# Optimization experiments

Measured on AMD Instinct MI355X. Metric: run time of the kernel, lower is better.

## Reference

```python
import jax, jax.numpy as jnp
import numpy as np

N_NODES = 50000
N_EDGES = 1_600_000
IN_DIM = 256
OUT_DIM = 128
NEG_SLOPE = 0.01  # F.leaky_relu default


def setup_inputs() -> dict:
    key = jax.random.key(0)
    k1, k2, k3, k4, k5 = jax.random.split(key, 5)
    x = jax.random.normal(k1, (N_NODES, IN_DIM), dtype=jnp.float32)
    # glorot_init: uniform in [-r, r], r = sqrt(6/(in+out))
    r = np.sqrt(6.0 / (IN_DIM + OUT_DIM)).astype(np.float32)
    weight = jax.random.uniform(k2, (IN_DIM, OUT_DIM), dtype=jnp.float32, minval=-r, maxval=r)
    adj_rows = jax.random.randint(k3, (N_EDGES,), 0, N_NODES, dtype=jnp.int64 if jax.config.jax_enable_x64 else jnp.int32)
    adj_cols = jax.random.randint(k4, (N_EDGES,), 0, N_NODES, dtype=jnp.int64 if jax.config.jax_enable_x64 else jnp.int32)
    adj_vals = jax.random.uniform(k5, (N_EDGES,), dtype=jnp.float32)
    return {"x": x, "weight": weight, "adj_vals": adj_vals,
            "adj_rows": adj_rows, "adj_cols": adj_cols}


def reference(x, weight, adj_vals, adj_rows, adj_cols):
    # h = X @ W : [N, OUT_DIM]
    h = x @ weight
    # sparse adj @ h via edge-list SpMM: out[r] += v * h[c]
    msgs = adj_vals[:, None] * h[adj_cols]            # [E, OUT_DIM]
    agg = jax.ops.segment_sum(msgs, adj_rows, num_segments=N_NODES)
    # leaky_relu epilogue
    return jnp.where(agg >= 0, agg, NEG_SLOPE * agg)
```

## Files before the change

kernel.cpp:

```cpp
#include <hip/hip_runtime.h>
#include <hip/hip_fp16.h>

#define N_NODES 50000
#define N_EDGES 1600000
#define IN_DIM 256
#define OUT_DIM 128
#define NEG_SLOPE 0.01f

#define SB_SH     10
#define NSB       49
#define BIN_SH    5
#define BIN_ROWS  32
#define NBIN_PAD  (NSB * 32)
#define NPART     8
#define ECAP      4608
#define SEGP      256
#define CAPG      (NPART * SEGP)
#define OVF_CAP   65536

#define SCAT_BLOCKS 256
#define EPB_S (N_EDGES / SCAT_BLOCKS)
#define SCAT_ITERS ((EPB_S + 511) / 512)

#define BM 128
#define GEMM_BLOCKS ((N_NODES + BM - 1) / BM)
#define PREP_BLOCKS (SCAT_BLOCKS + GEMM_BLOCKS + 1)

typedef _Float16 f16x8 __attribute__((ext_vector_type(8)));
typedef float    f32x4 __attribute__((ext_vector_type(4)));
typedef float    f32x8 __attribute__((ext_vector_type(8)));

__device__ __forceinline__ float lrelu(float v) {
    return v >= 0.f ? v : NEG_SLOPE * v;
}

#define CVT16(lo, hi) do { \
    lo[0]=(_Float16)xr[0].x; lo[1]=(_Float16)xr[0].y; lo[2]=(_Float16)xr[0].z; lo[3]=(_Float16)xr[0].w; \
    lo[4]=(_Float16)xr[1].x; lo[5]=(_Float16)xr[1].y; lo[6]=(_Float16)xr[1].z; lo[7]=(_Float16)xr[1].w; \
    hi[0]=(_Float16)xr[2].x; hi[1]=(_Float16)xr[2].y; hi[2]=(_Float16)xr[2].z; hi[3]=(_Float16)xr[2].w; \
    hi[4]=(_Float16)xr[3].x; hi[5]=(_Float16)xr[3].y; hi[6]=(_Float16)xr[3].z; hi[7]=(_Float16)xr[3].w; \
} while (0)

__global__ __launch_bounds__(512, 2) void prep(const int* __restrict__ rows,
                                               const int* __restrict__ cols,
                                               const float* __restrict__ vals,
                                               const float* __restrict__ x,
                                               const float* __restrict__ w,
                                               int* __restrict__ cstartarr,
                                               int* __restrict__ ovfcnt,
                                               int2* __restrict__ cbuf,
                                               __half* __restrict__ h) {
    __shared__ __attribute__((aligned(16))) char smem[50432];
    const int bid = blockIdx.x;
    const int t   = threadIdx.x;

    if (bid >= SCAT_BLOCKS + GEMM_BLOCKS) {
        if (t == 0) *ovfcnt = 0;
        return;
    }

    if (bid < SCAT_BLOCKS) {
        int2* lsort  = (int2*)smem;
        int*  hist   = (int*)(smem + 50000);
        int*  cstart = (int*)(smem + 50200);
        const int lane  = t & 63;
        const int blk   = bid;
        const int ebase = blk * EPB_S;

        if (t < NSB) hist[t] = 0;
        __syncthreads();

        int myr[SCAT_ITERS];
#pragma unroll
        for (int k = 0; k < SCAT_ITERS; ++k) {
            const int i = k * 512 + t;
            myr[k] = -1;
            if (i < EPB_S) {
                myr[k] = rows[ebase + i];
                atomicAdd(&hist[myr[k] >> SB_SH], 1);
            }
        }
        __syncthreads();

        if (t < 64) {
            const int v = (t < NSB) ? hist[t] : 0;
            int s = v;
#pragma unroll
            for (int off = 1; off < 64; off <<= 1) {
                const int u = __shfl_up(s, off);
                if (lane >= off) s += u;
            }
            if (t < NSB) { cstart[t] = s - v; hist[t] = s - v; }
        }
        __syncthreads();

#pragma unroll
        for (int k = 0; k < SCAT_ITERS; ++k) {
            const int i = k * 512 + t;
            if (i < EPB_S) {
                const int e = ebase + i;
                const int r = myr[k];
                const int pos = atomicAdd(&hist[r >> SB_SH], 1);
                lsort[pos] = make_int2((int)(((unsigned)r << 16) | (unsigned)cols[e]),
                                       __float_as_int(vals[e]));
            }
        }
        __syncthreads();

        {
            const int4* src = (const int4*)lsort;
            int4* dst = (int4*)(cbuf + (size_t)blk * EPB_S);
            for (int i = t; i < EPB_S / 2; i += 512) dst[i] = src[i];
        }
        if (t < NSB)  cstartarr[blk * 50 + t]   = cstart[t];
        if (t == NSB) cstartarr[blk * 50 + NSB] = EPB_S;
        return;
    }

    f16x8* wt8h = (f16x8*)smem;
    f16x8* xs8  = (f16x8*)(smem + 32768);
    const int a256 = (t < 256);
    const int lane = t & 63;
    const int wv   = t >> 6;
    const int row0 = (bid - SCAT_BLOCKS) * BM;

    const int srow = t >> 1;
    const int skh  = t & 1;
    const int grow = row0 + srow;
    const bool rv  = a256 && (grow < N_NODES);
    const float* xp = x + (size_t)(rv ? grow : 0) * IN_DIM + skh * 16;

    float4 xr[4];
    if (a256) {
#pragma unroll
        for (int i = 0; i < 4; ++i)
            xr[i] = rv ? ((const float4*)xp)[i] : make_float4(0.f, 0.f, 0.f, 0.f);
        f16x8 lo, hi;
        CVT16(lo, hi);
        xs8[(0 * 4 + skh * 2 + 0) * 128 + srow] = lo;
        xs8[(0 * 4 + skh * 2 + 1) * 128 + srow] = hi;
    }
    __syncthreads();

    f32x4 acc[2][8];
#pragma unroll
    for (int mf = 0; mf < 2; ++mf)
#pragma unroll
        for (int nf = 0; nf < 8; ++nf) acc[mf][nf] = (f32x4){0.f, 0.f, 0.f, 0.f};

    const int kgl = lane >> 4;
    const int l15 = lane & 15;
    const int mb  = (wv << 5) + l15;

#pragma unroll
    for (int H = 0; H < 2; ++H) {
        if (a256) {
#pragma unroll
            for (int itr = 0; itr < 8; ++itr) {
                const int e  = itr * 2048 + t * 8;
                const int kl = e >> 7;
                const int n0 = e & 127;
                const float4 a4 = *(const float4*)(w + (size_t)((H << 7) + kl) * 128 + n0);
                const float4 b4 = *(const float4*)(w + (size_t)((H << 7) + kl) * 128 + n0 + 4);
                __half* d = (__half*)wt8h + (size_t)(((kl >> 3) << 7) + n0) * 8 + (kl & 7);
                d[0]  = __float2half(a4.x);
                d[8]  = __float2half(a4.y);
                d[16] = __float2half(a4.z);
                d[24] = __float2half(a4.w);
                d[32] = __float2half(b4.x);
                d[40] = __float2half(b4.y);
                d[48] = __float2half(b4.z);
                d[56] = __float2half(b4.w);
            }
        }
        __syncthreads();

#pragma unroll
        for (int ksl = 0; ksl < 4; ++ksl) {
            const int ks  = H * 4 + ksl;
            const int cur = ks & 1;
            if (a256 && ks < 7) {
#pragma unroll
                for (int i = 0; i < 4; ++i)
                    xr[i] = rv ? ((const float4*)(xp + (ks + 1) * 32))[i]
                               : make_float4(0.f, 0.f, 0.f, 0.f);
            }
            if (a256) {
                const f16x8 b0 = xs8[(cur * 4 + kgl) * 128 + mb];
                const f16x8 b1 = xs8[(cur * 4 + kgl) * 128 + mb + 16];
                const int abase = ((ksl * 4 + kgl) << 7) + l15;
#pragma unroll
                for (int nf = 0; nf < 8; ++nf) {
                    const f16x8 a = wt8h[abase + (nf << 4)];
                    acc[0][nf] = __builtin_amdgcn_mfma_f32_16x16x32_f16(a, b0, acc[0][nf], 0, 0, 0);
                    acc[1][nf] = __builtin_amdgcn_mfma_f32_16x16x32_f16(a, b1, acc[1][nf], 0, 0, 0);
                }
            }
            if (a256 && ks < 7) {
                f16x8 lo, hi;
                CVT16(lo, hi);
                xs8[((cur ^ 1) * 4 + skh * 2 + 0) * 128 + srow] = lo;
                xs8[((cur ^ 1) * 4 + skh * 2 + 1) * 128 + srow] = hi;
            }
            __syncthreads();
        }
    }

    if (a256) {
        const int rg = lane >> 4;
#pragma unroll
        for (int mf = 0; mf < 2; ++mf) {
            const int m = row0 + (wv << 5) + (mf << 4) + l15;
            if (m < N_NODES) {
                __half* hp = h + (size_t)m * OUT_DIM + (rg << 2);
#pragma unroll
                for (int nf = 0; nf < 8; ++nf) {
                    union { ushort4 u; __half f[4]; } o;
                    o.f[0] = __float2half(acc[mf][nf][0]);
                    o.f[1] = __float2half(acc[mf][nf][1]);
                    o.f[2] = __float2half(acc[mf][nf][2]);
                    o.f[3] = __float2half(acc[mf][nf][3]);
                    *(ushort4*)(hp + (nf << 4)) = o.u;
                }
            }
        }
    }
}

__global__ __launch_bounds__(512) void scatter_fine(const int* __restrict__ cstartarr,
                                                    int* __restrict__ fs,
                                                    int* __restrict__ fc,
                                                    int* __restrict__ ovfcnt,
                                                    const int2* __restrict__ cbuf,
                                                    int2* __restrict__ ebuf,
                                                    int2* __restrict__ ovfbuf) {
    __shared__ int2 lsort[ECAP];
    __shared__ int  hist[32], cstart[32], fcv[32];
    __shared__ int  scnt[32], sstart[32];
    __shared__ int  stot;

    const int t    = threadIdx.x;
    const int lane = t & 63;
    const int wv   = t >> 6;
    const int sb   = blockIdx.x / NPART;
    const int p    = blockIdx.x % NPART;

    if (t < 32) {
        const int blk = p * 32 + t;
        const int s0 = cstartarr[blk * 50 + sb];
        const int s1 = cstartarr[blk * 50 + sb + 1];
        scnt[t]   = s1 - s0;
        sstart[t] = blk * EPB_S + s0;
        hist[t]   = 0;
    }
    __syncthreads();

    for (int j = 0; j < 4; ++j) {
        const int s = (wv << 2) + j;
        const int c = scnt[s];
        const int base = sstart[s];
        for (int i = lane; i < c; i += 64)
            atomicAdd(&hist[(cbuf[base + i].x >> 21) & 31], 1);
    }
    __syncthreads();

    if (t < 32) {
        const int v = hist[t];
        int s = v;
#pragma unroll
        for (int off = 1; off < 32; off <<= 1) {
            const int u = __shfl_up(s, off);
            if (t >= off) s += u;
        }
        if (t == 31) stot = s;
        cstart[t] = s - v;
        hist[t]   = s - v;
    }
    __syncthreads();

    for (int j = 0; j < 4; ++j) {
        const int s = (wv << 2) + j;
        const int c = scnt[s];
        const int base = sstart[s];
        for (int i = lane; i < c; i += 64) {
            const int2 rc = cbuf[base + i];
            const int fb = (rc.x >> 21) & 31;
            const int pos = atomicAdd(&hist[fb], 1);
            const int lrow = (rc.x >> 16) & 31;
            if (pos < ECAP) {
                lsort[pos] = make_int2((rc.x & 0xFFFF) | (lrow << 16) | (fb << 21), rc.y);
            } else {
                const int q = atomicAdd(ovfcnt, 1);
                if (q < OVF_CAP) ovfbuf[q] = rc;
            }
        }
    }
    __syncthreads();

    if (t < 32) {
        int c = hist[t] - cstart[t];
        if (c > SEGP) c = SEGP;
        if (cstart[t] + c > ECAP) c = (cstart[t] < ECAP) ? (ECAP - cstart[t]) : 0;
        fcv[t] = c;
        fs[(sb * 32 + t) * NPART + p] = cstart[t];
        fc[(sb * 32 + t) * NPART + p] = c;
    }
    __syncthreads();

    const int tot = min(stot, ECAP);
    int2* dst = ebuf + (size_t)(sb * NPART + p) * ECAP;
    for (int i = t; i < tot; i += 512) {
        const int2 rc = lsort[i];
        dst[i] = rc;
        const int fb  = (rc.x >> 21) & 31;
        const int off = i - cstart[fb];
        if (off >= fcv[fb]) {
            const int q = atomicAdd(ovfcnt, 1);
            if (q < OVF_CAP) {
                const int row = (sb << SB_SH) | (fb << BIN_SH) | ((rc.x >> 16) & 31);
                ovfbuf[q] = make_int2((int)(((unsigned)row << 16) | (unsigned)(rc.x & 0xFFFF)), rc.y);
            }
        }
    }
}

#define NCLS 256

#define STAGE(IT, HV, VV) do {                                                  \
    _Pragma("unroll")                                                           \
    for (int q = 0; q < 4; ++q) {                                               \
        const int idx = beg[q] + ((IT) << 2) + grp;                             \
        const bool vld = idx < end[q];                                          \
        const int2 r = srec[vld ? idx : last];                                  \
        VV[q] = vld ? __int_as_float(r.y) : 0.f;                                \
        HV[q] = *(const f16x8*)(h + (size_t)(r.x & 0xFFFF) * OUT_DIM + (gl << 3)); \
    }                                                                           \
} while (0)

__global__ __launch_bounds__(512, 4) void sort_gather(const int* __restrict__ fs,
                                                      const int* __restrict__ fc,
                                                      const int* __restrict__ ovfcnt,
                                                      const int2* __restrict__ ebuf,
                                                      const int2* __restrict__ ovfbuf,
                                                      const __half* __restrict__ h,
                                                      float* __restrict__ out) {
    __shared__ int2 urec[CAPG];
    __shared__ int2 srec[CAPG];
    __shared__ int  hist[NCLS];
    __shared__ int  pfx[NCLS];
    __shared__ int  rowoff_l[BIN_ROWS + 1];
    __shared__ int  wsum[4];
    __shared__ int  poff[NPART + 1];
    __shared__ int  fsrt[NPART];

    const int t    = threadIdx.x;
    const int bin  = blockIdx.x;
    const int wv   = t >> 6;
    const int lane = t & 63;
    const int sb   = bin >> 5;

    if (t < NCLS) hist[t] = 0;
    if (t < NPART) fsrt[t] = fs[bin * NPART + t];
    if (t == 0) {
        int a = 0;
        poff[0] = 0;
#pragma unroll
        for (int p = 0; p < NPART; ++p) { a += fc[bin * NPART + p]; poff[p + 1] = a; }
    }
    __syncthreads();
    const int cnt = poff[NPART];

    {
        const int cp = poff[wv + 1] - poff[wv];
        const int2* src = ebuf + (size_t)(sb * NPART + wv) * ECAP + fsrt[wv];
        const int ub = poff[wv];
        for (int i = lane; i < cp; i += 64) {
            const int2 r = src[i];
            urec[ub + i] = r;
            atomicAdd(&hist[(((r.x >> 16) & 31) << 3) | ((r.x & 0xFFFF) >> 13)], 1);
        }
    }
    __syncthreads();

    {
        const int v = (t < NCLS) ? hist[t] : 0;
        int s = v;
#pragma unroll
        for (int off = 1; off < 64; off <<= 1) {
            const int u = __shfl_up(s, off);
            if (lane >= off) s += u;
        }
        if (t < NCLS && lane == 63) wsum[wv] = s;
        __syncthreads();
        if (t == 0) {
            int a = 0;
#pragma unroll
            for (int i = 0; i < 4; ++i) { const int c = wsum[i]; wsum[i] = a; a += c; }
        }
        __syncthreads();
        if (t < NCLS) {
            const int incl = s + wsum[wv];
            pfx[t]  = incl;
            hist[t] = incl - v;
        }
    }
    __syncthreads();
    if (t < BIN_ROWS) rowoff_l[t] = t ? pfx[(t << 3) - 1] : 0;
    if (t == BIN_ROWS) rowoff_l[BIN_ROWS] = cnt;
    __syncthreads();

    for (int i = t; i < cnt; i += 512) {
        const int2 r = urec[i];
        const int cls = (((r.x >> 16) & 31) << 3) | ((r.x & 0xFFFF) >> 13);
        const int pos = atomicAdd(&hist[cls], 1);
        srec[pos] = r;
    }
    __syncthreads();

    const int grp = lane >> 4;
    const int gl  = lane & 15;
    const int r0  = wv << 2;
    const int last = cnt > 0 ? cnt - 1 : 0;

    int beg[4], end[4];
#pragma unroll
    for (int q = 0; q < 4; ++q) { beg[q] = rowoff_l[r0 + q]; end[q] = rowoff_l[r0 + q + 1]; }
    int nmax = 0;
#pragma unroll
    for (int q = 0; q < 4; ++q) nmax = max(nmax, end[q] - beg[q]);
    const int iters = (nmax + 3) >> 2;

    f32x8 acc[4];
#pragma unroll
    for (int q = 0; q < 4; ++q) acc[q] = (f32x8){0.f,0.f,0.f,0.f,0.f,0.f,0.f,0.f};

    if (cnt > 0 && iters > 0) {
        f16x8 hc[4], hn[4];
        float vc[4], vn[4];
        STAGE(0, hc, vc);
        for (int it = 0; it < iters; ++it) {
            const int itn = (it + 1 < iters) ? it + 1 : it;
            STAGE(itn, hn, vn);
            __builtin_amdgcn_sched_barrier(0);
#pragma unroll
            for (int q = 0; q < 4; ++q)
#pragma unroll
                for (int j = 0; j < 8; ++j) acc[q][j] += vc[q] * (float)hc[q][j];
            __builtin_amdgcn_sched_barrier(0);
#pragma unroll
            for (int q = 0; q < 4; ++q) { hc[q] = hn[q]; vc[q] = vn[q]; }
        }
    }

    int novf = *ovfcnt;
    if (novf > OVF_CAP) novf = OVF_CAP;
    for (int e = 0; e < novf; ++e) {
        const int2 rec = ovfbuf[e];
        const unsigned urow = ((unsigned)rec.x) >> 16;
        if ((int)(urow >> BIN_SH) == bin && grp == 0) {
            const int lr = (int)(urow & (BIN_ROWS - 1)) - r0;
            if (lr >= 0 && lr < 4) {
                const float v = __int_as_float(rec.y);
                const f16x8 hv = *(const f16x8*)(h + (size_t)(rec.x & 0xFFFF) * OUT_DIM + (gl << 3));
#pragma unroll
                for (int q = 0; q < 4; ++q)
                    if (q == lr)
#pragma unroll
                        for (int j = 0; j < 8; ++j) acc[q][j] += v * (float)hv[j];
            }
        }
    }

#pragma unroll
    for (int q = 0; q < 4; ++q)
#pragma unroll
        for (int j = 0; j < 8; ++j) {
            float x = acc[q][j];
            x += __shfl_xor(x, 16);
            x += __shfl_xor(x, 32);
            acc[q][j] = x;
        }

    float res[8];
#pragma unroll
    for (int j = 0; j < 8; ++j) {
        float x = acc[0][j];
        x = (grp == 1) ? acc[1][j] : x;
        x = (grp == 2) ? acc[2][j] : x;
        x = (grp == 3) ? acc[3][j] : x;
        res[j] = lrelu(x);
    }
    const int grow = (bin << BIN_SH) + r0 + grp;
    if (grow < N_NODES) {
        float* op = out + (size_t)grow * OUT_DIM + (gl << 3);
        *(float4*)op       = make_float4(res[0], res[1], res[2], res[3]);
        *(float4*)(op + 4) = make_float4(res[4], res[5], res[6], res[7]);
    }
}

extern "C" void kernel_launch(void* const* d_in, const int* in_sizes, int n_in,
                              void* d_out, int out_size, void* d_ws, size_t ws_size,
                              hipStream_t stream) {
    const float* x    = (const float*)d_in[0];
    const float* w    = (const float*)d_in[1];
    const float* vals = (const float*)d_in[2];
    const int*   rows = (const int*)d_in[3];
    const int*   cols = (const int*)d_in[4];
    float* out = (float*)d_out;

    char* ws = (char*)d_ws;
    size_t off = 0;
    auto alloc = [&](size_t bytes) {
        void* p = ws + off;
        off = (off + bytes + 255) & ~(size_t)255;
        return p;
    };
    int2*   cbuf     = (int2*)  alloc((size_t)N_EDGES * sizeof(int2));
    __half* h        = (__half*)alloc((size_t)N_NODES * OUT_DIM * sizeof(__half));
    int2*   ebuf     = (int2*)  alloc((size_t)NSB * NPART * ECAP * sizeof(int2));
    int2*   ovfbuf   = (int2*)  alloc((size_t)OVF_CAP * sizeof(int2));
    int*    cstartarr= (int*)   alloc((size_t)SCAT_BLOCKS * 50 * sizeof(int));
    int*    fs       = (int*)   alloc((size_t)NBIN_PAD * NPART * sizeof(int));
    int*    fc       = (int*)   alloc((size_t)NBIN_PAD * NPART * sizeof(int));
    int*    ovfcnt   = (int*)   alloc(sizeof(int));

    prep<<<PREP_BLOCKS, 512, 0, stream>>>(rows, cols, vals, x, w,
                                          cstartarr, ovfcnt, cbuf, h);
    scatter_fine<<<NSB * NPART, 512, 0, stream>>>(cstartarr, fs, fc, ovfcnt,
                                                  cbuf, ebuf, ovfbuf);
    sort_gather<<<NBIN_PAD, 512, 0, stream>>>(fs, fc, ovfcnt, ebuf, ovfbuf, h, out);
}
```

Measured before the change: 202.7 us.

## Halve row bins, double partitions, and simplify the gather stage

Row bins shrink from 32 to 16 rows, with twice as many partitions and smaller per-partition capacities. The gather kernel drops to 256 threads and drops its unsorted LDS staging buffer, reading the edge buffer from global memory twice (once for the histogram, once for the scatter). Each wave now handles two rows at a time instead of four, with no register prefetch stage. The aim is smaller LDS footprint, higher occupancy and less per-block imbalance, at the cost of losing software pipelining and doing extra global reads.

Result: faster. 192.5 us (-5.0%).

```diff
diff --git a/kernel.cpp b/kernel.cpp
--- a/kernel.cpp
+++ b/kernel.cpp
@@ -9,12 +9,12 @@
 
 #define SB_SH     10
 #define NSB       49
-#define BIN_SH    5
-#define BIN_ROWS  32
-#define NBIN_PAD  (NSB * 32)
-#define NPART     8
-#define ECAP      4608
-#define SEGP      256
+#define BIN_SH    4
+#define BIN_ROWS  16
+#define NBIN_PAD  (NSB * 64)
+#define NPART     16
+#define ECAP      2560
+#define SEGP      96
 #define CAPG      (NPART * SEGP)
 #define OVF_CAP   65536
 
@@ -235,8 +235,8 @@
                                                     int2* __restrict__ ebuf,
                                                     int2* __restrict__ ovfbuf) {
     __shared__ int2 lsort[ECAP];
-    __shared__ int  hist[32], cstart[32], fcv[32];
-    __shared__ int  scnt[32], sstart[32];
+    __shared__ int  hist[64], cstart[64], fcv[64];
+    __shared__ int  scnt[16], sstart[16];
     __shared__ int  stot;
 
     const int t    = threadIdx.x;
@@ -245,50 +245,49 @@
     const int sb   = blockIdx.x / NPART;
     const int p    = blockIdx.x % NPART;
 
-    if (t < 32) {
-        const int blk = p * 32 + t;
+    if (t < 16) {
+        const int blk = p * 16 + t;
         const int s0 = cstartarr[blk * 50 + sb];
         const int s1 = cstartarr[blk * 50 + sb + 1];
         scnt[t]   = s1 - s0;
         sstart[t] = blk * EPB_S + s0;
-        hist[t]   = 0;
-    }
-    __syncthreads();
-
-    for (int j = 0; j < 4; ++j) {
-        const int s = (wv << 2) + j;
+    }
+    if (t < 64) hist[t] = 0;
+    __syncthreads();
+
+    for (int j = 0; j < 2; ++j) {
+        const int s = (wv << 1) | j;
         const int c = scnt[s];
         const int base = sstart[s];
         for (int i = lane; i < c; i += 64)
-            atomicAdd(&hist[(cbuf[base + i].x >> 21) & 31], 1);
-    }
-    __syncthreads();
-
-    if (t < 32) {
+            atomicAdd(&hist[((unsigned)cbuf[base + i].x >> 20) & 63], 1);
+    }
+    __syncthreads();
+
+    if (t < 64) {
         const int v = hist[t];
         int s = v;
 #pragma unroll
-        for (int off = 1; off < 32; off <<= 1) {
+        for (int off = 1; off < 64; off <<= 1) {
             const int u = __shfl_up(s, off);
             if (t >= off) s += u;
         }
-        if (t == 31) stot = s;
+        if (t == 63) stot = s;
         cstart[t] = s - v;
         hist[t]   = s - v;
     }
     __syncthreads();
 
-    for (int j = 0; j < 4; ++j) {
-        const int s = (wv << 2) + j;
+    for (int j = 0; j < 2; ++j) {
+        const int s = (wv << 1) | j;
         const int c = scnt[s];
         const int base = sstart[s];
         for (int i = lane; i < c; i += 64) {
             const int2 rc = cbuf[base + i];
-            const int fb = (rc.x >> 21) & 31;
+            const int fb = ((unsigned)rc.x >> 20) & 63;
             const int pos = atomicAdd(&hist[fb], 1);
-            const int lrow = (rc.x >> 16) & 31;
             if (pos < ECAP) {
-                lsort[pos] = make_int2((rc.x & 0xFFFF) | (lrow << 16) | (fb << 21), rc.y);
+                lsort[pos] = rc;
             } else {
                 const int q = atomicAdd(ovfcnt, 1);
                 if (q < OVF_CAP) ovfbuf[q] = rc;
@@ -297,13 +296,13 @@
     }
     __syncthreads();
 
-    if (t < 32) {
+    if (t < 64) {
         int c = hist[t] - cstart[t];
         if (c > SEGP) c = SEGP;
         if (cstart[t] + c > ECAP) c = (cstart[t] < ECAP) ? (ECAP - cstart[t]) : 0;
         fcv[t] = c;
-        fs[(sb * 32 + t) * NPART + p] = cstart[t];
-        fc[(sb * 32 + t) * NPART + p] = c;
+        fs[(sb * 64 + t) * NPART + p] = cstart[t];
+        fc[(sb * 64 + t) * NPART + p] = c;
     }
     __syncthreads();
 
@@ -312,39 +311,24 @@
     for (int i = t; i < tot; i += 512) {
         const int2 rc = lsort[i];
         dst[i] = rc;
-        const int fb  = (rc.x >> 21) & 31;
+        const int fb  = ((unsigned)rc.x >> 20) & 63;
         const int off = i - cstart[fb];
         if (off >= fcv[fb]) {
             const int q = atomicAdd(ovfcnt, 1);
-            if (q < OVF_CAP) {
-                const int row = (sb << SB_SH) | (fb << BIN_SH) | ((rc.x >> 16) & 31);
-                ovfbuf[q] = make_int2((int)(((unsigned)row << 16) | (unsigned)(rc.x & 0xFFFF)), rc.y);
-            }
+            if (q < OVF_CAP) ovfbuf[q] = rc;
         }
     }
 }
 
 #define NCLS 256
 
-#define STAGE(IT, HV, VV) do {                                                  \
-    _Pragma("unroll")                                                           \
-    for (int q = 0; q < 4; ++q) {                                               \
-        const int idx = beg[q] + ((IT) << 2) + grp;                             \
-        const bool vld = idx < end[q];                                          \
-        const int2 r = srec[vld ? idx : last];                                  \
-        VV[q] = vld ? __int_as_float(r.y) : 0.f;                                \
-        HV[q] = *(const f16x8*)(h + (size_t)(r.x & 0xFFFF) * OUT_DIM + (gl << 3)); \
-    }                                                                           \
-} while (0)
-
-__global__ __launch_bounds__(512, 4) void sort_gather(const int* __restrict__ fs,
-                                                      const int* __restrict__ fc,
-                                                      const int* __restrict__ ovfcnt,
-                                                      const int2* __restrict__ ebuf,
-                                                      const int2* __restrict__ ovfbuf,
-                                                      const __half* __restrict__ h,
-                                                      float* __restrict__ out) {
-    __shared__ int2 urec[CAPG];
+__global__ __launch_bounds__(256) void sort_gather(const int* __restrict__ fs,
+                                                   const int* __restrict__ fc,
+                                                   const int* __restrict__ ovfcnt,
+                                                   const int2* __restrict__ ebuf,
+                                                   const int2* __restrict__ ovfbuf,
+                                                   const __half* __restrict__ h,
+                                                   float* __restrict__ out) {
     __shared__ int2 srec[CAPG];
     __shared__ int  hist[NCLS];
     __shared__ int  pfx[NCLS];
@@ -357,9 +341,9 @@
     const int bin  = blockIdx.x;
     const int wv   = t >> 6;
     const int lane = t & 63;
-    const int sb   = bin >> 5;
-
-    if (t < NCLS) hist[t] = 0;
+    const int sb   = bin >> 6;
+
+    hist[t] = 0;
     if (t < NPART) fsrt[t] = fs[bin * NPART + t];
     if (t == 0) {
         int a = 0;
@@ -370,27 +354,27 @@
     __syncthreads();
     const int cnt = poff[NPART];
 
+#pragma unroll
+    for (int j = 0; j < 4; ++j) {
+        const int p  = (wv << 2) + j;
+        const int cp = poff[p + 1] - poff[p];
+        const int2* src = ebuf + (size_t)(sb * NPART + p) * ECAP + fsrt[p];
+        for (int i = lane; i < cp; i += 64) {
+            const int k = src[i].x;
+            atomicAdd(&hist[(((k >> 16) & 15) << 4) | ((k & 0xFFFF) >> 12)], 1);
+        }
+    }
+    __syncthreads();
+
     {
-        const int cp = poff[wv + 1] - poff[wv];
-        const int2* src = ebuf + (size_t)(sb * NPART + wv) * ECAP + fsrt[wv];
-        const int ub = poff[wv];
-        for (int i = lane; i < cp; i += 64) {
-            const int2 r = src[i];
-            urec[ub + i] = r;
-            atomicAdd(&hist[(((r.x >> 16) & 31) << 3) | ((r.x & 0xFFFF) >> 13)], 1);
-        }
-    }
-    __syncthreads();
-
-    {
-        const int v = (t < NCLS) ? hist[t] : 0;
+        const int v = hist[t];
         int s = v;
 #pragma unroll
         for (int off = 1; off < 64; off <<= 1) {
             const int u = __shfl_up(s, off);
             if (lane >= off) s += u;
         }
-        if (t < NCLS && lane == 63) wsum[wv] = s;
+        if (lane == 63) wsum[wv] = s;
         __syncthreads();
         if (t == 0) {
             int a = 0;
@@ -398,103 +382,102 @@
             for (int i = 0; i < 4; ++i) { const int c = wsum[i]; wsum[i] = a; a += c; }
         }
         __syncthreads();
-        if (t < NCLS) {
-            const int incl = s + wsum[wv];
-            pfx[t]  = incl;
-            hist[t] = incl - v;
-        }
-    }
-    __syncthreads();
-    if (t < BIN_ROWS) rowoff_l[t] = t ? pfx[(t << 3) - 1] : 0;
+        const int incl = s + wsum[wv];
+        pfx[t]  = incl;
+        hist[t] = incl - v;
+    }
+    __syncthreads();
+    if (t < BIN_ROWS) rowoff_l[t] = t ? pfx[(t << 4) - 1] : 0;
     if (t == BIN_ROWS) rowoff_l[BIN_ROWS] = cnt;
     __syncthreads();
 
-    for (int i = t; i < cnt; i += 512) {
-        const int2 r = urec[i];
-        const int cls = (((r.x >> 16) & 31) << 3) | ((r.x & 0xFFFF) >> 13);
-        const int pos = atomicAdd(&hist[cls], 1);
-        srec[pos] = r;
+#pragma unroll
+    for (int j = 0; j < 4; ++j) {
+        const int p  = (wv << 2) + j;
+        const int cp = poff[p + 1] - poff[p];
+        const int2* src = ebuf + (size_t)(sb * NPART + p) * ECAP + fsrt[p];
+        for (int i = lane; i < cp; i += 64) {
+            const int2 r = src[i];
+            const int cls = (((r.x >> 16) & 15) << 4) | ((r.x & 0xFFFF) >> 12);
+            const int pos = atomicAdd(&hist[cls], 1);
+            srec[pos] = r;
+        }
     }
     __syncthreads();
 
     const int grp = lane >> 4;
     const int gl  = lane & 15;
-    const int r0  = wv << 2;
-    const int last = cnt > 0 ? cnt - 1 : 0;
-
-    int beg[4], end[4];
-#pragma unroll
-    for (int q = 0; q < 4; ++q) { beg[q] = rowoff_l[r0 + q]; end[q] = rowoff_l[r0 + q + 1]; }
-    int nmax = 0;
-#pragma unroll
-    for (int q = 0; q < 4; ++q) nmax = max(nmax, end[q] - beg[q]);
-    const int iters = (nmax + 3) >> 2;
-
-    f32x8 acc[4];
-#pragma unroll
-    for (int q = 0; q < 4; ++q) acc[q] = (f32x8){0.f,0.f,0.f,0.f,0.f,0.f,0.f,0.f};
-
-    if (cnt > 0 && iters > 0) {
-        f16x8 hc[4], hn[4];
-        float vc[4], vn[4];
-        STAGE(0, hc, vc);
-        for (int it = 0; it < iters; ++it) {
-            const int itn = (it + 1 < iters) ? it + 1 : it;
-            STAGE(itn, hn, vn);
-            __builtin_amdgcn_sched_barrier(0);
-#pragma unroll
-            for (int q = 0; q < 4; ++q)
-#pragma unroll
-                for (int j = 0; j < 8; ++j) acc[q][j] += vc[q] * (float)hc[q][j];
-            __builtin_amdgcn_sched_barrier(0);
-#pragma unroll
-            for (int q = 0; q < 4; ++q) { hc[q] = hn[q]; vc[q] = vn[q]; }
-        }
-    }
-
     int novf = *ovfcnt;
     if (novf > OVF_CAP) novf = OVF_CAP;
-    for (int e = 0; e < novf; ++e) {
-        const int2 rec = ovfbuf[e];
-        const unsigned urow = ((unsigned)rec.x) >> 16;
-        if ((int)(urow >> BIN_SH) == bin && grp == 0) {
-            const int lr = (int)(urow & (BIN_ROWS - 1)) - r0;
-            if (lr >= 0 && lr < 4) {
-                const float v = __int_as_float(rec.y);
-                const f16x8 hv = *(const f16x8*)(h + (size_t)(rec.x & 0xFFFF) * OUT_DIM + (gl << 3));
-#pragma unroll
-                for (int q = 0; q < 4; ++q)
-                    if (q == lr)
-#pragma unroll
-                        for (int j = 0; j < 8; ++j) acc[q][j] += v * (float)hv[j];
-            }
-        }
-    }
-
-#pragma unroll
-    for (int q = 0; q < 4; ++q)
+
+    for (int pp = 0; pp < 2; ++pp) {
+        const int lr0 = (wv << 2) + 2 * pp;
+        const int lr1 = lr0 + 1;
+        const int b0 = rowoff_l[lr0], e0 = rowoff_l[lr0 + 1];
+        const int b1 = rowoff_l[lr1], e1 = rowoff_l[lr1 + 1];
+        const int n0 = e0 - b0, n1 = e1 - b1;
+        const int nmax = n0 > n1 ? n0 : n1;
+        const int iters = (nmax + 3) >> 2;
+
+        f32x8 a0 = (f32x8){0.f,0.f,0.f,0.f,0.f,0.f,0.f,0.f};
+        f32x8 a1 = (f32x8){0.f,0.f,0.f,0.f,0.f,0.f,0.f,0.f};
+
+        for (int it = 0; it < iters; ++it) {
+            const int i0 = b0 + (it << 2) + grp;
+            const int i1 = b1 + (it << 2) + grp;
+            const bool v0i = i0 < e0;
+            const bool v1i = i1 < e1;
+            const int2 rA = srec[v0i ? i0 : 0];
+            const int2 rB = srec[v1i ? i1 : 0];
+            const float vA = v0i ? __int_as_float(rA.y) : 0.f;
+            const float vB = v1i ? __int_as_float(rB.y) : 0.f;
+            const f16x8 hA = *(const f16x8*)(h + (size_t)(rA.x & 0xFFFF) * OUT_DIM + (gl << 3));
+            const f16x8 hB = *(const f16x8*)(h + (size_t)(rB.x & 0xFFFF) * OUT_DIM + (gl << 3));
+#pragma unroll
+            for (int j = 0; j < 8; ++j) {
+                a0[j] += vA * (float)hA[j];
+                a1[j] += vB * (float)hB[j];
+            }
+        }
+
+        for (int e = 0; e < novf; ++e) {
+            const int2 rec = ovfbuf[e];
+            const unsigned urow = ((unsigned)rec.x) >> 16;
+            if ((int)(urow >> BIN_SH) == bin && grp == 0) {
+                const int lr = (int)(urow & (BIN_ROWS - 1));
+                if (lr == lr0 || lr == lr1) {
+                    const float v = __int_as_float(rec.y);
+                    const f16x8 hv = *(const f16x8*)(h + (size_t)(rec.x & 0xFFFF) * OUT_DIM + (gl << 3));
+#pragma unroll
+                    for (int j = 0; j < 8; ++j) {
+                        if (lr == lr0) a0[j] += v * (float)hv[j];
+                        else           a1[j] += v * (float)hv[j];
+                    }
+                }
+            }
+        }
+
 #pragma unroll
         for (int j = 0; j < 8; ++j) {
-            float x = acc[q][j];
-            x += __shfl_xor(x, 16);
-            x += __shfl_xor(x, 32);
-            acc[q][j] = x;
-        }
-
-    float res[8];
-#pragma unroll
-    for (int j = 0; j < 8; ++j) {
-        float x = acc[0][j];
-        x = (grp == 1) ? acc[1][j] : x;
-        x = (grp == 2) ? acc[2][j] : x;
-        x = (grp == 3) ? acc[3][j] : x;
-        res[j] = lrelu(x);
-    }
-    const int grow = (bin << BIN_SH) + r0 + grp;
-    if (grow < N_NODES) {
-        float* op = out + (size_t)grow * OUT_DIM + (gl << 3);
-        *(float4*)op       = make_float4(res[0], res[1], res[2], res[3]);
-        *(float4*)(op + 4) = make_float4(res[4], res[5], res[6], res[7]);
+            float x0 = a0[j], x1 = a1[j];
+            x0 += __shfl_xor(x0, 16); x0 += __shfl_xor(x0, 32);
+            x1 += __shfl_xor(x1, 16); x1 += __shfl_xor(x1, 32);
+            a0[j] = x0; a1[j] = x1;
+        }
+
+        const int lrow = (grp & 2) ? lr1 : lr0;
+        const int grow = (bin << BIN_SH) + lrow;
+        float q[4];
+#pragma unroll
+        for (int k = 0; k < 4; ++k) {
+            const float lo = (grp & 2) ? a1[k]     : a0[k];
+            const float hi = (grp & 2) ? a1[k + 4] : a0[k + 4];
+            q[k] = lrelu((grp & 1) ? hi : lo);
+        }
+        if (grow < N_NODES) {
+            float4 o = make_float4(q[0], q[1], q[2], q[3]);
+            *(float4*)(out + (size_t)grow * OUT_DIM + (gl << 3) + ((grp & 1) << 2)) = o;
+        }
     }
 }
 
@@ -528,5 +511,5 @@
                                           cstartarr, ovfcnt, cbuf, h);
     scatter_fine<<<NSB * NPART, 512, 0, stream>>>(cstartarr, fs, fc, ovfcnt,
                                                   cbuf, ebuf, ovfbuf);
-    sort_gather<<<NBIN_PAD, 512, 0, stream>>>(fs, fc, ovfcnt, ebuf, ovfbuf, h, out);
+    sort_gather<<<NBIN_PAD, 256, 0, stream>>>(fs, fc, ovfcnt, ebuf, ovfbuf, h, out);
 }
```
